# Optimization experiments

Measured on AMD Instinct MI355X. Metric: run time of the kernel, lower is better.

The kernel has to match this reference:

```python
import jax, jax.numpy as jnp
import numpy as np

B, S, D_MODEL, D_K, D_V, N_HEAD = 2, 2048, 1024, 1024, 1024, 16


def setup_inputs() -> dict:
    key = jax.random.key(0)
    k1, k2, k3, k4, k5, k6, k7 = jax.random.split(key, 7)
    s = 1.0 / np.sqrt(D_MODEL)
    return {
        "q": jax.random.normal(k1, (B, S, D_MODEL), dtype=jnp.float32),
        "k": jax.random.normal(k2, (B, S, D_MODEL), dtype=jnp.float32),
        "v": jax.random.normal(k3, (B, S, D_MODEL), dtype=jnp.float32),
        "Wq": jax.random.normal(k4, (D_MODEL, D_K), dtype=jnp.float32) * s,
        "Wk": jax.random.normal(k5, (D_MODEL, D_K), dtype=jnp.float32) * s,
        "Wv": jax.random.normal(k6, (D_MODEL, D_V), dtype=jnp.float32) * s,
        "Wp": jax.random.normal(k7, (D_V, D_MODEL), dtype=jnp.float32) * (1.0 / np.sqrt(D_V)),
    }


def reference(q, k, v, Wq, Wk, Wv, Wp):
    b, sq, _ = q.shape
    sk = k.shape[1]
    hd_k = D_K // N_HEAD
    hd_v = D_V // N_HEAD
    # Faithful to original: plain row-major reshape (B,S,d) -> (B,H,S,d/H),
    # i.e. the sequence axis is split across heads (as torch .view does here).
    Q = (q @ Wq).reshape(b, N_HEAD, sq, hd_k)
    K = (k @ Wk).reshape(b, N_HEAD, sk, hd_k)
    V = (v @ Wv).reshape(b, N_HEAD, sk, hd_v)
    # No 1/sqrt(d_k) scaling in the original module.
    wei = jnp.einsum('bhqd,bhkd->bhqk', Q, K)
    # causal mask (masked=True): tril(ones(sq, sk))
    causal = jnp.arange(sq)[:, None] >= jnp.arange(sk)[None, :]
    wei = jnp.where(causal[None, None], wei, -jnp.inf)
    att = jnp.einsum('bhqk,bhkd->bhqd', jax.nn.softmax(wei, axis=-1), V)
    out = jnp.swapaxes(att, 1, 2).reshape(b, sq, D_V)
    return out @ Wp
```

## Files before the change

kernel.cpp:

```cpp
#include <hip/hip_runtime.h>
#include <cstdint>
#include <cstddef>


typedef _Float16 f16;
typedef _Float16 f16x8 __attribute__((ext_vector_type(8)));
typedef float f32x4 __attribute__((ext_vector_type(4)));

#define NB 2
#define NS 2048
#define NDM 1024
#define NHEAD 16

__device__ __forceinline__ void gload16(void* lds, const void* g) {
    __builtin_amdgcn_global_load_lds(
        (__attribute__((address_space(1))) void*)g,
        (__attribute__((address_space(3))) void*)lds, 16, 0, 0);
}

__device__ __forceinline__ float fast_exp2(float x) {
#if __has_builtin(__builtin_amdgcn_exp2f)
    return __builtin_amdgcn_exp2f(x);
#else
    return __expf(x * 0.69314718055994531f);
#endif
}

__global__ __launch_bounds__(256) void cast3_kernel(
    const float* __restrict__ s0, const float* __restrict__ s1, const float* __restrict__ s2,
    f16* __restrict__ d0, f16* __restrict__ d1, f16* __restrict__ d2, int nvec)
{
    const float* s = blockIdx.z == 0 ? s0 : (blockIdx.z == 1 ? s1 : s2);
    f16* d        = blockIdx.z == 0 ? d0 : (blockIdx.z == 1 ? d1 : d2);
    int vi = blockIdx.x * 256 + threadIdx.x;
    if (vi >= nvec) return;
    const float4* sp = (const float4*)s;
    float4 a = sp[vi * 2 + 0];
    float4 b = sp[vi * 2 + 1];
    f16x8 h;
    h[0] = (f16)a.x; h[1] = (f16)a.y; h[2] = (f16)a.z; h[3] = (f16)a.w;
    h[4] = (f16)b.x; h[5] = (f16)b.y; h[6] = (f16)b.z; h[7] = (f16)b.w;
    *(f16x8*)(d + (size_t)vi * 8) = h;
}

__global__ __launch_bounds__(256) void tcast4_kernel(
    const float* __restrict__ w0, const float* __restrict__ w1,
    const float* __restrict__ w2, const float* __restrict__ w3,
    f16* __restrict__ t0, f16* __restrict__ t1, f16* __restrict__ t2, f16* __restrict__ t3)
{
    const int n = 1024;
    const float* W; f16* T;
    switch (blockIdx.z) {
        case 0: W = w0; T = t0; break;
        case 1: W = w1; T = t1; break;
        case 2: W = w2; T = t2; break;
        default: W = w3; T = t3; break;
    }
    __shared__ float tile[32][33];
    int tx = threadIdx.x, ty = threadIdx.y;
    int c0 = blockIdx.x * 32, r0 = blockIdx.y * 32;
    #pragma unroll
    for (int i = 0; i < 32; i += 8)
        tile[ty + i][tx] = W[(size_t)(r0 + ty + i) * n + c0 + tx];
    __syncthreads();
    #pragma unroll
    for (int i = 0; i < 32; i += 8)
        T[(size_t)(c0 + ty + i) * n + r0 + tx] = (f16)tile[tx][ty + i];
}

template <typename CT>
__device__ __forceinline__ void gemm_abt_body(
    const f16* __restrict__ A, const f16* __restrict__ Bt, CT* __restrict__ C,
    int M, int N, int K, int bx, int by, float cscale)
{
    __shared__ f16 As[128][64];
    __shared__ f16 Bs[128][64];
    const int tid  = threadIdx.x;
    const int lane = tid & 63, wave = tid >> 6;
    const int quad = lane >> 4, ln = lane & 15;
    const int wm = wave >> 1, wn = wave & 1;
    const int m0 = by * 128, n0 = bx * 128;
    const int r8 = lane >> 3, c8 = lane & 7;
    const int swz = ((c8 ^ r8) * 8);

    f32x4 acc[4][4] = {};
    for (int k0 = 0; k0 < K; k0 += 64) {
        __syncthreads();
        #pragma unroll
        for (int i = 0; i < 4; i++) {
            int blk = wave * 4 + i;
            int row = blk * 8 + r8;
            gload16(&As[blk * 8][0], &A [(size_t)(m0 + row) * K + k0 + swz]);
            gload16(&Bs[blk * 8][0], &Bt[(size_t)(n0 + row) * K + k0 + swz]);
        }
        __syncthreads();
        #pragma unroll
        for (int kc = 0; kc < 2; kc++) {
            f16x8 af[4], bfr[4];
            #pragma unroll
            for (int mt = 0; mt < 4; mt++)
                af[mt] = *(const f16x8*)&As[wm * 64 + mt * 16 + ln][((kc * 4 + quad) ^ (ln & 7)) * 8];
            #pragma unroll
            for (int nt = 0; nt < 4; nt++)
                bfr[nt] = *(const f16x8*)&Bs[wn * 64 + nt * 16 + ln][((kc * 4 + quad) ^ (ln & 7)) * 8];
            #pragma unroll
            for (int mt = 0; mt < 4; mt++)
                #pragma unroll
                for (int nt = 0; nt < 4; nt++)
                    acc[mt][nt] = __builtin_amdgcn_mfma_f32_16x16x32_f16(af[mt], bfr[nt], acc[mt][nt], 0, 0, 0);
        }
    }
    #pragma unroll
    for (int mt = 0; mt < 4; mt++)
        #pragma unroll
        for (int nt = 0; nt < 4; nt++)
            #pragma unroll
            for (int r = 0; r < 4; r++) {
                int row = m0 + wm * 64 + mt * 16 + quad * 4 + r;
                int col = n0 + wn * 64 + nt * 16 + ln;
                C[(size_t)row * N + col] = (CT)(acc[mt][nt][r] * cscale);
            }
}

__global__ __launch_bounds__(256) void gemm3_kernel(
    const f16* __restrict__ a0, const f16* __restrict__ a1, const f16* __restrict__ a2,
    const f16* __restrict__ b0, const f16* __restrict__ b1, const f16* __restrict__ b2,
    f16* __restrict__ c0, f16* __restrict__ c1, f16* __restrict__ c2, int M, int N, int K)
{
    const f16 *A, *Bt; f16* C; float sc;
    switch (blockIdx.z) {
        case 0: A = a0; Bt = b0; C = c0; sc = 1.4426950408889634f; break;
        case 1: A = a1; Bt = b1; C = c1; sc = 1.0f; break;
        default: A = a2; Bt = b2; C = c2; sc = 1.0f; break;
    }
    gemm_abt_body<f16>(A, Bt, C, M, N, K, blockIdx.x, blockIdx.y, sc);
}

__global__ __launch_bounds__(256) void gemm_out_kernel(
    const f16* __restrict__ A, const f16* __restrict__ Bt, float* __restrict__ C, int M, int N, int K)
{
    gemm_abt_body<float>(A, Bt, C, M, N, K, blockIdx.x, blockIdx.y, 1.0f);
}

__global__ __launch_bounds__(256) void vtrans_kernel(
    const f16* __restrict__ Vp, f16* __restrict__ Vt)
{
    const int kt = blockIdx.x;
    const int h  = blockIdx.y;
    const int b  = blockIdx.z;
    const f16* src = Vp + (size_t)b * (NS * NDM) + (size_t)h * (128 * NDM);
    f16* dst = Vt + (size_t)(b * NHEAD + h) * (64 * 2048);

    __shared__ f16 Ls[64][64];
    const int tid = threadIdx.x;
    #pragma unroll
    for (int i = 0; i < 2; i++) {
        int vi = tid + i * 256;
        int key = vi >> 3, c = vi & 7;
        int cs = c ^ ((key >> 3) & 7);
        *(uint4*)&Ls[key][cs * 8] = *(const uint4*)&src[(size_t)(kt * 64 + key) * 64 + c * 8];
    }
    __syncthreads();
    #pragma unroll
    for (int i = 0; i < 2; i++) {
        int vi = tid + i * 256;
        int d2 = vi >> 3, kc = vi & 7;
        int cs = (d2 >> 3) ^ kc;
        f16 tmp[8];
        #pragma unroll
        for (int j = 0; j < 8; j++)
            tmp[j] = Ls[kc * 8 + j][cs * 8 + (d2 & 7)];
        *(uint4*)&dst[(size_t)d2 * 2048 + kt * 64 + kc * 8] = *(uint4*)tmp;
    }
}

__global__ __launch_bounds__(256) void attn_kernel(
    const f16* __restrict__ Qp, const f16* __restrict__ Kp, const f16* __restrict__ Vt,
    f16* __restrict__ att)
{
    const int p = blockIdx.x;
    const int h = blockIdx.y;
    const int b = blockIdx.z;
    const size_t hb = (size_t)b * (NS * NDM) + (size_t)h * (128 * NDM);
    const f16* Qh = Qp + hb;
    const f16* Kh = Kp + hb;
    const f16* Vh = Vt + (size_t)(b * NHEAD + h) * (64 * 2048);

    __shared__ f16 PQ[64][136];
    __shared__ f16 Ks[128][64];
    __shared__ f16 Vs[64][128];

    const int tid  = threadIdx.x;
    const int lane = tid & 63, wave = tid >> 6;
    const int quad = lane >> 4, ln = lane & 15;
    const int r8 = lane >> 3, c8 = lane & 7;
    const int r4 = lane >> 4, c16 = lane & 15;

    for (int pass = 0; pass < 2; pass++) {
        const int qt = pass == 0 ? (31 - p) : p;
        __syncthreads();
        #pragma unroll
        for (int i = 0; i < 2; i++) {
            int vi = tid + i * 256;
            int row = vi >> 3, kk = (vi & 7) * 8;
            *(uint4*)&PQ[row][kk] = *(const uint4*)&Qh[(size_t)(qt * 64 + row) * 64 + kk];
        }
        __syncthreads();
        f16x8 qf[2];
        #pragma unroll
        for (int kc = 0; kc < 2; kc++)
            qf[kc] = *(const f16x8*)&PQ[wave * 16 + ln][kc * 32 + quad * 8];

        float m_i[4], l_i[4];
        #pragma unroll
        for (int r = 0; r < 4; r++) { m_i[r] = -3e30f; l_i[r] = 0.f; }
        f32x4 o[4] = {};

        const int nkt = (qt + 2) >> 1;
        for (int kt = 0; kt < nkt; kt++) {
            __syncthreads();
            #pragma unroll
            for (int i = 0; i < 4; i++) {
                int blk = wave * 4 + i;
                int krow = blk * 8 + r8;
                gload16(&Ks[blk * 8][0], &Kh[(size_t)(kt * 128 + krow) * 64 + ((c8 ^ r8) * 8)]);
                int vrow = blk * 4 + r4;
                gload16(&Vs[blk * 4][0], &Vh[(size_t)vrow * 2048 + kt * 128 + ((c16 ^ (vrow & 15)) * 8)]);
            }
            __syncthreads();

            f32x4 sf[8] = {};
            #pragma unroll
            for (int kc = 0; kc < 2; kc++)
                #pragma unroll
                for (int ct = 0; ct < 8; ct++) {
                    int krow = ct * 16 + ln;
                    f16x8 kf = *(const f16x8*)&Ks[krow][((kc * 4 + quad) ^ (ln & 7)) * 8];
                    sf[ct] = __builtin_amdgcn_mfma_f32_16x16x32_f16(qf[kc], kf, sf[ct], 0, 0, 0);
                }

            if (kt == nkt - 1) {
                #pragma unroll
                for (int ct = 0; ct < 8; ct++) {
                    int jg = kt * 128 + ct * 16 + ln;
                    #pragma unroll
                    for (int r = 0; r < 4; r++) {
                        int ig = qt * 64 + wave * 16 + quad * 4 + r;
                        if (jg > ig) sf[ct][r] = -3e30f;
                    }
                }
            }

            float alpha[4];
            #pragma unroll
            for (int r = 0; r < 4; r++) {
                float tm = sf[0][r];
                #pragma unroll
                for (int ct = 1; ct < 8; ct++) tm = fmaxf(tm, sf[ct][r]);
                #pragma unroll
                for (int off = 1; off < 16; off <<= 1) tm = fmaxf(tm, __shfl_xor(tm, off, 64));
                float mnew = fmaxf(m_i[r], tm);
                float a = fast_exp2(m_i[r] - mnew);
                float rs = 0.f;
                #pragma unroll
                for (int ct = 0; ct < 8; ct++) {
                    float pv = fast_exp2(sf[ct][r] - mnew);
                    sf[ct][r] = pv; rs += pv;
                }
                #pragma unroll
                for (int off = 1; off < 16; off <<= 1) rs += __shfl_xor(rs, off, 64);
                m_i[r] = mnew; l_i[r] = l_i[r] * a + rs; alpha[r] = a;
            }
            #pragma unroll
            for (int vt = 0; vt < 4; vt++)
                #pragma unroll
                for (int r = 0; r < 4; r++) o[vt][r] *= alpha[r];

            #pragma unroll
            for (int ct = 0; ct < 8; ct++)
                #pragma unroll
                for (int r = 0; r < 4; r++)
                    PQ[wave * 16 + quad * 4 + r][ct * 16 + ln] = (f16)sf[ct][r];

            #pragma unroll
            for (int kc = 0; kc < 4; kc++) {
                f16x8 pa = *(const f16x8*)&PQ[wave * 16 + ln][kc * 32 + quad * 8];
                #pragma unroll
                for (int vt = 0; vt < 4; vt++) {
                    int vrow = vt * 16 + ln;
                    f16x8 vb = *(const f16x8*)&Vs[vrow][(((kc * 4 + quad) ^ ln) & 15) * 8];
                    o[vt] = __builtin_amdgcn_mfma_f32_16x16x32_f16(pa, vb, o[vt], 0, 0, 0);
                }
            }
        }

        #pragma unroll
        for (int r = 0; r < 4; r++) {
            float inv = 1.0f / l_i[r];
            int s2 = qt * 64 + wave * 16 + quad * 4 + r;
            #pragma unroll
            for (int vt = 0; vt < 4; vt++) {
                int d2 = vt * 16 + ln;
                att[((size_t)b * NS + s2) * NDM + h * 64 + d2] = (f16)(o[vt][r] * inv);
            }
        }
    }
}

extern "C" void kernel_launch(void* const* d_in, const int* in_sizes, int n_in,
                              void* d_out, int out_size, void* d_ws, size_t ws_size,
                              hipStream_t stream)
{
    const float* q  = (const float*)d_in[0];
    const float* k  = (const float*)d_in[1];
    const float* v  = (const float*)d_in[2];
    const float* Wq = (const float*)d_in[3];
    const float* Wk = (const float*)d_in[4];
    const float* Wv = (const float*)d_in[5];
    const float* Wp = (const float*)d_in[6];
    float* out = (float*)d_out;

    char* ws = (char*)d_ws;
    const size_t MB = 1024 * 1024;
    f16* qb   = (f16*)(ws + 0 * MB);
    f16* kb   = (f16*)(ws + 8 * MB);
    f16* vb   = (f16*)(ws + 16 * MB);
    f16* Wqt  = (f16*)(ws + 24 * MB);
    f16* Wkt  = (f16*)(ws + 26 * MB);
    f16* Wvt  = (f16*)(ws + 28 * MB);
    f16* Wpt  = (f16*)(ws + 30 * MB);
    f16* Qp   = (f16*)(ws + 32 * MB);
    f16* Kp   = (f16*)(ws + 40 * MB);
    f16* Vp   = (f16*)(ws + 48 * MB);
    f16* attb = (f16*)(ws + 56 * MB);
    f16* Vtg  = vb;

    const int M = NB * NS;
    const int N = NDM;
    const int K = NDM;

    cast3_kernel<<<dim3(2048, 1, 3), 256, 0, stream>>>(q, k, v, qb, kb, vb, (M * NDM) / 8);
    tcast4_kernel<<<dim3(32, 32, 4), dim3(32, 8), 0, stream>>>(Wq, Wk, Wv, Wp, Wqt, Wkt, Wvt, Wpt);
    gemm3_kernel<<<dim3(N / 128, M / 128, 3), 256, 0, stream>>>(qb, kb, vb, Wqt, Wkt, Wvt, Qp, Kp, Vp, M, N, K);
    vtrans_kernel<<<dim3(32, NHEAD, NB), 256, 0, stream>>>(Vp, Vtg);
    attn_kernel<<<dim3(16, NHEAD, NB), 256, 0, stream>>>(Qp, Kp, Vtg, attb);
    gemm_out_kernel<<<dim3(N / 128, M / 128, 1), 256, 0, stream>>>(attb, Wpt, out, M, N, K);
}
```

Measured before the change: 235.4 us.

## Merge prep kernels, retile output GEMM, compute softmax row sums via MFMA

Merges the input-cast and weight-transpose-cast kernels into one launch, which removes a kernel launch. The output projection GEMM moves to 128x64 tiles, doubling its block count from 256 to 512 so more CUs are busy on this small problem. In attention, the per-row sum reduction with shuffles is replaced by an extra MFMA against a vector of ones, so the rowsum is taken from the fp16-rounded probabilities. This trades shuffle and ALU work for one more MFMA per k-chunk.

Measured after the change: 239.7 us. About the same (+1.8%).

```diff
diff --git a/kernel.cpp b/kernel.cpp
--- a/kernel.cpp
+++ b/kernel.cpp
@@ -26,46 +26,48 @@
 #endif
 }
 
-__global__ __launch_bounds__(256) void cast3_kernel(
-    const float* __restrict__ s0, const float* __restrict__ s1, const float* __restrict__ s2,
-    f16* __restrict__ d0, f16* __restrict__ d1, f16* __restrict__ d2, int nvec)
-{
-    const float* s = blockIdx.z == 0 ? s0 : (blockIdx.z == 1 ? s1 : s2);
-    f16* d        = blockIdx.z == 0 ? d0 : (blockIdx.z == 1 ? d1 : d2);
-    int vi = blockIdx.x * 256 + threadIdx.x;
-    if (vi >= nvec) return;
-    const float4* sp = (const float4*)s;
-    float4 a = sp[vi * 2 + 0];
-    float4 b = sp[vi * 2 + 1];
-    f16x8 h;
-    h[0] = (f16)a.x; h[1] = (f16)a.y; h[2] = (f16)a.z; h[3] = (f16)a.w;
-    h[4] = (f16)b.x; h[5] = (f16)b.y; h[6] = (f16)b.z; h[7] = (f16)b.w;
-    *(f16x8*)(d + (size_t)vi * 8) = h;
-}
-
-__global__ __launch_bounds__(256) void tcast4_kernel(
+__global__ __launch_bounds__(256) void prep_kernel(
+    const float* __restrict__ q, const float* __restrict__ k, const float* __restrict__ v,
+    f16* __restrict__ qb, f16* __restrict__ kb, f16* __restrict__ vb,
     const float* __restrict__ w0, const float* __restrict__ w1,
     const float* __restrict__ w2, const float* __restrict__ w3,
     f16* __restrict__ t0, f16* __restrict__ t1, f16* __restrict__ t2, f16* __restrict__ t3)
 {
-    const int n = 1024;
-    const float* W; f16* T;
-    switch (blockIdx.z) {
-        case 0: W = w0; T = t0; break;
-        case 1: W = w1; T = t1; break;
-        case 2: W = w2; T = t2; break;
-        default: W = w3; T = t3; break;
-    }
     __shared__ float tile[32][33];
-    int tx = threadIdx.x, ty = threadIdx.y;
-    int c0 = blockIdx.x * 32, r0 = blockIdx.y * 32;
-    #pragma unroll
-    for (int i = 0; i < 32; i += 8)
-        tile[ty + i][tx] = W[(size_t)(r0 + ty + i) * n + c0 + tx];
-    __syncthreads();
-    #pragma unroll
-    for (int i = 0; i < 32; i += 8)
-        T[(size_t)(c0 + ty + i) * n + r0 + tx] = (f16)tile[tx][ty + i];
+    const int bx = blockIdx.x, tid = threadIdx.x;
+    if (bx < 6144) {
+        const int arr = bx >> 11;
+        const float* s = arr == 0 ? q : (arr == 1 ? k : v);
+        f16* d        = arr == 0 ? qb : (arr == 1 ? kb : vb);
+        int vi = (bx & 2047) * 256 + tid;
+        const float4* sp = (const float4*)s;
+        float4 a = sp[vi * 2 + 0];
+        float4 b = sp[vi * 2 + 1];
+        f16x8 h;
+        h[0] = (f16)a.x; h[1] = (f16)a.y; h[2] = (f16)a.z; h[3] = (f16)a.w;
+        h[4] = (f16)b.x; h[5] = (f16)b.y; h[6] = (f16)b.z; h[7] = (f16)b.w;
+        *(f16x8*)(d + (size_t)vi * 8) = h;
+    } else {
+        const int t = bx - 6144;
+        const int mat = t >> 10, tl = t & 1023;
+        const float* W; f16* T;
+        switch (mat) {
+            case 0: W = w0; T = t0; break;
+            case 1: W = w1; T = t1; break;
+            case 2: W = w2; T = t2; break;
+            default: W = w3; T = t3; break;
+        }
+        const int n = 1024;
+        const int tx = tid & 31, ty = tid >> 5;
+        const int c0 = (tl & 31) * 32, r0 = (tl >> 5) * 32;
+        #pragma unroll
+        for (int i = 0; i < 32; i += 8)
+            tile[ty + i][tx] = W[(size_t)(r0 + ty + i) * n + c0 + tx];
+        __syncthreads();
+        #pragma unroll
+        for (int i = 0; i < 32; i += 8)
+            T[(size_t)(c0 + ty + i) * n + r0 + tx] = (f16)tile[tx][ty + i];
+    }
 }
 
 template <typename CT>
@@ -137,9 +139,58 @@
 }
 
 __global__ __launch_bounds__(256) void gemm_out_kernel(
-    const f16* __restrict__ A, const f16* __restrict__ Bt, float* __restrict__ C, int M, int N, int K)
-{
-    gemm_abt_body<float>(A, Bt, C, M, N, K, blockIdx.x, blockIdx.y, 1.0f);
+    const f16* __restrict__ A, const f16* __restrict__ Bt, float* __restrict__ C,
+    int M, int N, int K)
+{
+    __shared__ f16 As[128][64];
+    __shared__ f16 Bs[64][64];
+    const int tid  = threadIdx.x;
+    const int lane = tid & 63, wave = tid >> 6;
+    const int quad = lane >> 4, ln = lane & 15;
+    const int m0 = blockIdx.y * 128, n0 = blockIdx.x * 64;
+    const int r8 = lane >> 3, c8 = lane & 7;
+    const int swz = ((c8 ^ r8) * 8);
+
+    f32x4 acc[2][4] = {};
+    for (int k0 = 0; k0 < K; k0 += 64) {
+        __syncthreads();
+        #pragma unroll
+        for (int i = 0; i < 4; i++) {
+            int blk = wave * 4 + i;
+            gload16(&As[blk * 8][0], &A[(size_t)(m0 + blk * 8 + r8) * K + k0 + swz]);
+        }
+        #pragma unroll
+        for (int i = 0; i < 2; i++) {
+            int blk = wave * 2 + i;
+            gload16(&Bs[blk * 8][0], &Bt[(size_t)(n0 + blk * 8 + r8) * K + k0 + swz]);
+        }
+        __syncthreads();
+        #pragma unroll
+        for (int kc = 0; kc < 2; kc++) {
+            f16x8 af[2], bfr[4];
+            #pragma unroll
+            for (int mt = 0; mt < 2; mt++)
+                af[mt] = *(const f16x8*)&As[wave * 32 + mt * 16 + ln][((kc * 4 + quad) ^ (ln & 7)) * 8];
+            #pragma unroll
+            for (int nt = 0; nt < 4; nt++)
+                bfr[nt] = *(const f16x8*)&Bs[nt * 16 + ln][((kc * 4 + quad) ^ (ln & 7)) * 8];
+            #pragma unroll
+            for (int mt = 0; mt < 2; mt++)
+                #pragma unroll
+                for (int nt = 0; nt < 4; nt++)
+                    acc[mt][nt] = __builtin_amdgcn_mfma_f32_16x16x32_f16(af[mt], bfr[nt], acc[mt][nt], 0, 0, 0);
+        }
+    }
+    #pragma unroll
+    for (int mt = 0; mt < 2; mt++)
+        #pragma unroll
+        for (int nt = 0; nt < 4; nt++)
+            #pragma unroll
+            for (int r = 0; r < 4; r++) {
+                int row = m0 + wave * 32 + mt * 16 + quad * 4 + r;
+                int col = n0 + nt * 16 + ln;
+                C[(size_t)row * N + col] = acc[mt][nt][r];
+            }
 }
 
 __global__ __launch_bounds__(256) void vtrans_kernel(
@@ -196,6 +247,10 @@
     const int r8 = lane >> 3, c8 = lane & 7;
     const int r4 = lane >> 4, c16 = lane & 15;
 
+    f16x8 ones;
+    #pragma unroll
+    for (int j = 0; j < 8; j++) ones[j] = (f16)1.0f;
+
     for (int pass = 0; pass < 2; pass++) {
         const int qt = pass == 0 ? (31 - p) : p;
         __syncthreads();
@@ -211,10 +266,11 @@
         for (int kc = 0; kc < 2; kc++)
             qf[kc] = *(const f16x8*)&PQ[wave * 16 + ln][kc * 32 + quad * 8];
 
-        float m_i[4], l_i[4];
-        #pragma unroll
-        for (int r = 0; r < 4; r++) { m_i[r] = -3e30f; l_i[r] = 0.f; }
+        float m_i[4];
+        #pragma unroll
+        for (int r = 0; r < 4; r++) m_i[r] = -3e30f;
         f32x4 o[4] = {};
+        f32x4 o5 = {};
 
         const int nkt = (qt + 2) >> 1;
         for (int kt = 0; kt < nkt; kt++) {
@@ -251,7 +307,6 @@
                 }
             }
 
-            float alpha[4];
             #pragma unroll
             for (int r = 0; r < 4; r++) {
                 float tm = sf[0][r];
@@ -261,20 +316,14 @@
                 for (int off = 1; off < 16; off <<= 1) tm = fmaxf(tm, __shfl_xor(tm, off, 64));
                 float mnew = fmaxf(m_i[r], tm);
                 float a = fast_exp2(m_i[r] - mnew);
-                float rs = 0.f;
-                #pragma unroll
-                for (int ct = 0; ct < 8; ct++) {
-                    float pv = fast_exp2(sf[ct][r] - mnew);
-                    sf[ct][r] = pv; rs += pv;
-                }
-                #pragma unroll
-                for (int off = 1; off < 16; off <<= 1) rs += __shfl_xor(rs, off, 64);
-                m_i[r] = mnew; l_i[r] = l_i[r] * a + rs; alpha[r] = a;
-            }
-            #pragma unroll
-            for (int vt = 0; vt < 4; vt++)
-                #pragma unroll
-                for (int r = 0; r < 4; r++) o[vt][r] *= alpha[r];
+                m_i[r] = mnew;
+                #pragma unroll
+                for (int ct = 0; ct < 8; ct++)
+                    sf[ct][r] = fast_exp2(sf[ct][r] - mnew);
+                #pragma unroll
+                for (int vt = 0; vt < 4; vt++) o[vt][r] *= a;
+                o5[r] *= a;
+            }
 
             #pragma unroll
             for (int ct = 0; ct < 8; ct++)
@@ -291,12 +340,13 @@
                     f16x8 vb = *(const f16x8*)&Vs[vrow][(((kc * 4 + quad) ^ ln) & 15) * 8];
                     o[vt] = __builtin_amdgcn_mfma_f32_16x16x32_f16(pa, vb, o[vt], 0, 0, 0);
                 }
+                o5 = __builtin_amdgcn_mfma_f32_16x16x32_f16(pa, ones, o5, 0, 0, 0);
             }
         }
 
         #pragma unroll
         for (int r = 0; r < 4; r++) {
-            float inv = 1.0f / l_i[r];
+            float inv = 1.0f / o5[r];
             int s2 = qt * 64 + wave * 16 + quad * 4 + r;
             #pragma unroll
             for (int vt = 0; vt < 4; vt++) {
@@ -339,10 +389,10 @@
     const int N = NDM;
     const int K = NDM;
 
-    cast3_kernel<<<dim3(2048, 1, 3), 256, 0, stream>>>(q, k, v, qb, kb, vb, (M * NDM) / 8);
-    tcast4_kernel<<<dim3(32, 32, 4), dim3(32, 8), 0, stream>>>(Wq, Wk, Wv, Wp, Wqt, Wkt, Wvt, Wpt);
+    prep_kernel<<<dim3(10240), 256, 0, stream>>>(q, k, v, qb, kb, vb,
+                                                 Wq, Wk, Wv, Wp, Wqt, Wkt, Wvt, Wpt);
     gemm3_kernel<<<dim3(N / 128, M / 128, 3), 256, 0, stream>>>(qb, kb, vb, Wqt, Wkt, Wvt, Qp, Kp, Vp, M, N, K);
     vtrans_kernel<<<dim3(32, NHEAD, NB), 256, 0, stream>>>(Vp, Vtg);
     attn_kernel<<<dim3(16, NHEAD, NB), 256, 0, stream>>>(Qp, Kp, Vtg, attb);
-    gemm_out_kernel<<<dim3(N / 128, M / 128, 1), 256, 0, stream>>>(attb, Wpt, out, M, N, K);
-}
+    gemm_out_kernel<<<dim3(N / 64, M / 128), 256, 0, stream>>>(attb, Wpt, out, M, N, K);
+}
```
